# Performance work log

Hardware: AMD Instinct MI355X
Metric: run time of the kernel (lower is better)

## Reference

```python
import jax, jax.numpy as jnp
import numpy as np

N_NODES = 100000
N_EDGES = 1200000
NUM_GRAPHS = 64
D_IN = 64
D_H = 64
D_OUT = 2
BN_EPS = 1e-5


def setup_inputs() -> dict:
    key = jax.random.key(0)
    ks = jax.random.split(key, 12)
    x = jax.random.normal(ks[0], (N_NODES, D_IN), dtype=jnp.float32)
    edge_index = jax.random.randint(ks[1], (2, N_EDGES), 0, N_NODES, dtype=jnp.int64 if jax.config.read('jax_enable_x64') else jnp.int32)
    batch = jnp.sort(jax.random.randint(ks[2], (N_NODES,), 0, NUM_GRAPHS))
    s = 1.0 / np.sqrt(D_H)
    W1 = jax.random.uniform(ks[3], (D_IN, D_H), minval=-s, maxval=s, dtype=jnp.float32)
    b1 = jnp.zeros((D_H,), jnp.float32)
    g1 = jnp.ones((D_H,), jnp.float32); be1 = jnp.zeros((D_H,), jnp.float32)
    m1 = jax.random.normal(ks[4], (D_H,), dtype=jnp.float32) * 0.1
    v1 = jax.random.uniform(ks[5], (D_H,), minval=0.5, maxval=1.5, dtype=jnp.float32)
    W2 = jax.random.uniform(ks[6], (D_H, D_H), minval=-s, maxval=s, dtype=jnp.float32)
    b2 = jnp.zeros((D_H,), jnp.float32)
    g2 = jnp.ones((D_H,), jnp.float32); be2 = jnp.zeros((D_H,), jnp.float32)
    m2 = jax.random.normal(ks[7], (D_H,), dtype=jnp.float32) * 0.1
    v2 = jax.random.uniform(ks[8], (D_H,), minval=0.5, maxval=1.5, dtype=jnp.float32)
    Wc = jax.random.uniform(ks[9], (D_H, D_OUT), minval=-s, maxval=s, dtype=jnp.float32)
    bc = jnp.zeros((D_OUT,), jnp.float32)
    return dict(x=x, edge_index=edge_index, batch=batch, W1=W1, b1=b1, g1=g1, be1=be1, m1=m1, v1=v1,
                W2=W2, b2=b2, g2=g2, be2=be2, m2=m2, v2=v2, Wc=Wc, bc=bc)


def _gcn_conv(x, src, dst, W, b):
    n = x.shape[0]
    h = x @ W  # [N, Dh]
    deg = jax.ops.segment_sum(jnp.ones_like(dst, dtype=h.dtype), dst, num_segments=n)  # includes self-loops
    dinv = jax.lax.rsqrt(jnp.maximum(deg, 1.0))
    norm = dinv[src] * dinv[dst]  # [E+N]
    msg = h[src] * norm[:, None]
    out = jax.ops.segment_sum(msg, dst, num_segments=n)
    return out + b


def _bn(x, g, be, m, v):
    return (x - m) * (g * jax.lax.rsqrt(v + BN_EPS)) + be


def reference(x, edge_index, batch, W1, b1, g1, be1, m1, v1, W2, b2, g2, be2, m2, v2, Wc, bc):
    n = x.shape[0]
    loop = jnp.arange(n, dtype=edge_index.dtype)
    src = jnp.concatenate([edge_index[0], loop])
    dst = jnp.concatenate([edge_index[1], loop])
    h = _gcn_conv(x, src, dst, W1, b1)
    h = jax.nn.relu(_bn(h, g1, be1, m1, v1))  # dropout is identity in eval
    h = _gcn_conv(h, src, dst, W2, b2)
    h = jax.nn.relu(_bn(h, g2, be2, m2, v2))
    # global mean pool over graphs
    sums = jax.ops.segment_sum(h, batch, num_segments=NUM_GRAPHS)
    cnts = jax.ops.segment_sum(jnp.ones((n,), h.dtype), batch, num_segments=NUM_GRAPHS)
    pooled = sums / jnp.maximum(cnts, 1.0)[:, None]
    return pooled @ Wc + bc
```

## Files before the change

### kernel.cpp

```cpp
#include <hip/hip_runtime.h>

#define N_NODES_C 100000
#define N_EDGES_C 1200000
#define NQUADS_C 300000
#define NUM_GRAPHS_C 64
#define D_C 64
#define BN_EPS_C 1e-5f

#define BU_SH 7
#define NB_C 782
#define PART_B 512
#define QPB 586

typedef unsigned short u16;
typedef unsigned int u32;

using frag_ab = __attribute__((ext_vector_type(8))) short;
using f32x4   = __attribute__((ext_vector_type(4))) float;

__device__ __forceinline__ u16 f2bf(float f) {
    u32 x = __float_as_uint(f);
    x += 0x7fffu + ((x >> 16) & 1u);
    return (u16)(x >> 16);
}
__device__ __forceinline__ float bf2f(u16 u) {
    return __uint_as_float(((u32)u) << 16);
}

__global__ void k_prep(const float* __restrict__ x,
                       const float* __restrict__ W1, const float* __restrict__ W2,
                       u16* __restrict__ Xb, u16* __restrict__ Wb1,
                       u16* __restrict__ Wb2, u16* __restrict__ T) {
    int i = blockIdx.x * 256 + threadIdx.x;
    int base = i * 4;
    if (base < N_NODES_C * D_C) {
        float4 f = *(const float4*)(x + base);
        ushort4 o;
        o.x = f2bf(f.x); o.y = f2bf(f.y); o.z = f2bf(f.z); o.w = f2bf(f.w);
        *(ushort4*)(Xb + base) = o;
    }
    if (i < 4096) {
        int n = i >> 6, k = i & 63;
        Wb1[i] = f2bf(W1[k * 64 + n]);
        Wb2[i] = f2bf(W2[k * 64 + n]);
    }
    if (i < 64) T[(size_t)N_NODES_C * 64 + i] = 0;
}


__global__ void __launch_bounds__(256) k_hist(const int* __restrict__ dst,
                                              u32* __restrict__ hist_all) {
    __shared__ u32 hist[NB_C];
    int b = blockIdx.x, t = threadIdx.x;
    for (int i = t; i < NB_C; i += 256) hist[i] = 0;
    __syncthreads();
    int qlo = b * QPB, qhi = qlo + QPB; if (qhi > NQUADS_C) qhi = NQUADS_C;
    const int4* d4 = (const int4*)dst;
    for (int i = qlo + t; i < qhi; i += 256) {
        int4 d = d4[i];
        atomicAdd(&hist[d.x >> BU_SH], 1u);
        atomicAdd(&hist[d.y >> BU_SH], 1u);
        atomicAdd(&hist[d.z >> BU_SH], 1u);
        atomicAdd(&hist[d.w >> BU_SH], 1u);
    }
    __syncthreads();
    for (int i = t; i < NB_C; i += 256) hist_all[(size_t)b * NB_C + i] = hist[i];
}

__global__ void __launch_bounds__(256) k_pscan(const u32* __restrict__ hist_all,
                                               u32* __restrict__ partLocal,
                                               u32* __restrict__ bucketTotal) {
    int wv = blockIdx.x * 4 + (threadIdx.x >> 6);
    int l = threadIdx.x & 63;
    if (wv >= NB_C) return;
    u32 v[8];
#pragma unroll
    for (int j = 0; j < 8; ++j) v[j] = hist_all[(size_t)(l * 8 + j) * NB_C + wv];
    u32 s = 0;
#pragma unroll
    for (int j = 0; j < 8; ++j) { u32 tv = v[j]; v[j] = s; s += tv; }
    u32 run = s;
#pragma unroll
    for (int off = 1; off < 64; off <<= 1) {
        u32 y = __shfl_up(run, off);
        if (l >= off) run += y;
    }
    u32 excl = run - s;
#pragma unroll
    for (int j = 0; j < 8; ++j)
        partLocal[(size_t)(l * 8 + j) * NB_C + wv] = excl + v[j];
    if (l == 63) bucketTotal[wv] = run;
}

__global__ void __launch_bounds__(1024) k_bscan(const u32* __restrict__ bucketTotal,
                                                u32* __restrict__ bucketStart) {
    __shared__ u32 sh[1024];
    int t = threadIdx.x;
    u32 c = (t < NB_C) ? bucketTotal[t] : 0;
    u32 val = c;
    sh[t] = val;
    __syncthreads();
#pragma unroll
    for (int off = 1; off < 1024; off <<= 1) {
        u32 y = (t >= off) ? sh[t - off] : 0;
        __syncthreads();
        val += y;
        sh[t] = val;
        __syncthreads();
    }
    if (t < NB_C) bucketStart[t] = val - c;
    if (t == 0) bucketStart[NB_C] = N_EDGES_C;
}

__global__ void __launch_bounds__(256) k_part(const int* __restrict__ src,
                                              const int* __restrict__ dst,
                                              const u32* __restrict__ partLocal,
                                              const u32* __restrict__ bucketStart,
                                              uint2* __restrict__ pairs) {
    __shared__ u32 baseLDS[NB_C];
    __shared__ u32 rank[NB_C];
    int b = blockIdx.x, t = threadIdx.x;
    for (int i = t; i < NB_C; i += 256) {
        baseLDS[i] = bucketStart[i] + partLocal[(size_t)b * NB_C + i];
        rank[i] = 0;
    }
    __syncthreads();
    int qlo = b * QPB, qhi = qlo + QPB; if (qhi > NQUADS_C) qhi = NQUADS_C;
    const int4* d4 = (const int4*)dst;
    const int4* s4 = (const int4*)src;
    for (int i = qlo + t; i < qhi; i += 256) {
        int4 d = d4[i];
        int4 s = s4[i];
        int dd[4] = {d.x, d.y, d.z, d.w};
        int ss[4] = {s.x, s.y, s.z, s.w};
#pragma unroll
        for (int k = 0; k < 4; ++k) {
            int bu = dd[k] >> BU_SH;
            u32 r = atomicAdd(&rank[bu], 1u);
            pairs[baseLDS[bu] + r] = make_uint2((u32)ss[k], (u32)dd[k]);
        }
    }
}

__global__ void __launch_bounds__(256) k_csr(const uint2* __restrict__ pairs,
                                             const u32* __restrict__ bucketStart,
                                             int* __restrict__ cnt,
                                             int* __restrict__ start,
                                             int* __restrict__ col) {
    __shared__ u32 cl[128];
    __shared__ u32 sl[128];
    __shared__ u32 rk[128];
    __shared__ int sh[256];
    int bu = blockIdx.x, t = threadIdx.x;
    int n0 = bu << BU_SH;
    u32 seg0 = bucketStart[bu], seg1 = bucketStart[bu + 1];
    if (t < 128) { cl[t] = 0; rk[t] = 0; }
    __syncthreads();
    for (u32 i = seg0 + t; i < seg1; i += 256)
        atomicAdd(&cl[pairs[i].y - n0], 1u);
    __syncthreads();
    int c = (t < 128) ? (int)cl[t] : 0;
    int val = c;
    sh[t] = val;
    __syncthreads();
#pragma unroll
    for (int off = 1; off < 128; off <<= 1) {
        int y = (t >= off) ? sh[t - off] : 0;
        __syncthreads();
        val += y;
        sh[t] = val;
        __syncthreads();
    }
    if (t < 128) {
        int node = n0 + t;
        u32 st = seg0 + (u32)(val - c);
        sl[t] = st;
        if (node < N_NODES_C) { cnt[node] = c; start[node] = (int)st; }
    }
    __syncthreads();
    for (u32 i = seg0 + t; i < seg1; i += 256) {
        uint2 pr = pairs[i];
        u32 loc = pr.y - n0;
        u32 r = atomicAdd(&rk[loc], 1u);
        col[sl[loc] + r] = (int)pr.x;
    }
}

__global__ void __launch_bounds__(256) k_gemm_mfma(
        const u16* __restrict__ Xb, const u16* __restrict__ Wb,
        const int* __restrict__ cnt, u16* __restrict__ T) {
    int lane = threadIdx.x & 63;
    int q = lane >> 4, ln = lane & 15;
    int wave = blockIdx.x * 4 + (threadIdx.x >> 6);
    int nwaves = gridDim.x * 4;
    frag_ab bfr[4][2];
#pragma unroll
    for (int nt = 0; nt < 4; ++nt)
#pragma unroll
        for (int kh = 0; kh < 2; ++kh)
            bfr[nt][kh] = *(const frag_ab*)(Wb + (nt * 16 + ln) * 64 + kh * 32 + q * 8);
    const int nstrips = N_NODES_C / 16;
    for (int s = wave; s < nstrips; s += nwaves) {
        int r0 = s * 16;
        frag_ab a0 = *(const frag_ab*)(Xb + (size_t)(r0 + ln) * 64 + q * 8);
        frag_ab a1 = *(const frag_ab*)(Xb + (size_t)(r0 + ln) * 64 + 32 + q * 8);
        f32x4 acc[4];
#pragma unroll
        for (int nt = 0; nt < 4; ++nt) {
            acc[nt] = (f32x4){0.f, 0.f, 0.f, 0.f};
            acc[nt] = __builtin_amdgcn_mfma_f32_16x16x32_bf16(a0, bfr[nt][0], acc[nt], 0, 0, 0);
            acc[nt] = __builtin_amdgcn_mfma_f32_16x16x32_bf16(a1, bfr[nt][1], acc[nt], 0, 0, 0);
        }
        float di[4];
#pragma unroll
        for (int reg = 0; reg < 4; ++reg)
            di[reg] = rsqrtf((float)(cnt[r0 + q * 4 + reg] + 1));
#pragma unroll
        for (int nt = 0; nt < 4; ++nt)
#pragma unroll
            for (int reg = 0; reg < 4; ++reg)
                T[(size_t)(r0 + q * 4 + reg) * 64 + nt * 16 + ln] =
                    f2bf(acc[nt][reg] * di[reg]);
    }
}

template <bool POOL>
__device__ __forceinline__ void gather_body(
        const u16* __restrict__ T, const int* __restrict__ col,
        const int* __restrict__ cnt, const int* __restrict__ start,
        const float* __restrict__ b, const float* __restrict__ g,
        const float* __restrict__ be, const float* __restrict__ m,
        const float* __restrict__ v, const int* __restrict__ batch,
        u16* __restrict__ Ab, float* __restrict__ pooled) {
    const int ZROW = N_NODES_C;
    int lane = threadIdx.x & 63;
    int h = lane >> 4, c = lane & 15;
    int cbase = c << 2;
    int wave = blockIdx.x * 4 + (threadIdx.x >> 6);
    int nwaves = gridDim.x * 4;
    float scv[4], c0v[4];
#pragma unroll
    for (int i = 0; i < 4; ++i) {
        float sci = g[cbase + i] * rsqrtf(v[cbase + i] + BN_EPS_C);
        scv[i] = sci;
        c0v[i] = (b[cbase + i] - m[cbase + i]) * sci + be[cbase + i];
    }
    const int chunk = (N_NODES_C + nwaves - 1) / nwaves;
    int p0 = wave * chunk;
    int p1 = p0 + chunk; if (p1 > N_NODES_C) p1 = N_NODES_C;
    if (p0 >= p1) return;

    float psum = 0.f; int curg = -1;

    int d0 = cnt[p0];
    int s0 = start[p0];
    int d1 = 0, s1 = 0;
    if (p0 + 1 < p1) { d1 = cnt[p0 + 1]; s1 = start[p0 + 1]; }
    int cv0 = col[(size_t)(u32)s0 + lane];

    for (int p = p0; p < p1; ++p) {
        int deg = __builtin_amdgcn_readfirstlane(d0);
        int cvR = cv0;
        if (p + 1 < p1) {
            cv0 = col[(size_t)(u32)s1 + lane];
            d0 = d1;
            if (p + 2 < p1) { d1 = cnt[p + 2]; s1 = start[p + 2]; }
        }
        if (deg > 63) deg = 63;
        int cv = (lane < deg) ? cvR : ((lane == deg) ? p : ZROW);
        int iters = (deg + 4) >> 2;
        float a0 = 0.f, a1 = 0.f, a2 = 0.f, a3 = 0.f;
        int sl = h;
        int j = 0;
        for (; j + 2 <= iters; j += 2) {
            int i0 = __shfl(cv, sl);
            int i1 = __shfl(cv, sl + 4);
            uint2 t0 = *(const uint2*)(T + (((size_t)(u32)i0) << 6) + (c << 2));
            uint2 t1 = *(const uint2*)(T + (((size_t)(u32)i1) << 6) + (c << 2));
            a0 += __uint_as_float(t0.x << 16); a1 += __uint_as_float(t0.x & 0xffff0000u);
            a2 += __uint_as_float(t0.y << 16); a3 += __uint_as_float(t0.y & 0xffff0000u);
            a0 += __uint_as_float(t1.x << 16); a1 += __uint_as_float(t1.x & 0xffff0000u);
            a2 += __uint_as_float(t1.y << 16); a3 += __uint_as_float(t1.y & 0xffff0000u);
            sl += 8;
        }
        if (j < iters) {
            int i0 = __shfl(cv, sl);
            uint2 t0 = *(const uint2*)(T + (((size_t)(u32)i0) << 6) + (c << 2));
            a0 += __uint_as_float(t0.x << 16); a1 += __uint_as_float(t0.x & 0xffff0000u);
            a2 += __uint_as_float(t0.y << 16); a3 += __uint_as_float(t0.y & 0xffff0000u);
        }
        a0 += __shfl_xor(a0, 16); a0 += __shfl_xor(a0, 32);
        a1 += __shfl_xor(a1, 16); a1 += __shfl_xor(a1, 32);
        a2 += __shfl_xor(a2, 16); a2 += __shfl_xor(a2, 32);
        a3 += __shfl_xor(a3, 16); a3 += __shfl_xor(a3, 32);
        float dr = rsqrtf((float)(deg + 1));
        if (POOL) {
            float asel = (h & 2) ? ((h & 1) ? a3 : a2) : ((h & 1) ? a1 : a0);
            float scl  = (h & 2) ? ((h & 1) ? scv[3] : scv[2]) : ((h & 1) ? scv[1] : scv[0]);
            float c0l  = (h & 2) ? ((h & 1) ? c0v[3] : c0v[2]) : ((h & 1) ? c0v[1] : c0v[0]);
            float vh = fmaxf(fmaf(asel * dr, scl, c0l), 0.f);
            int gg = batch[p];
            if (gg != curg) {
                if (curg >= 0) atomicAdd(&pooled[curg * 64 + cbase + h], psum);
                curg = gg; psum = 0.f;
            }
            psum += vh;
        } else {
            float v0 = fmaxf(fmaf(a0 * dr, scv[0], c0v[0]), 0.f);
            float v1 = fmaxf(fmaf(a1 * dr, scv[1], c0v[1]), 0.f);
            float v2 = fmaxf(fmaf(a2 * dr, scv[2], c0v[2]), 0.f);
            float v3 = fmaxf(fmaf(a3 * dr, scv[3], c0v[3]), 0.f);
            if (h == 0) {
                u32 w0 = (u32)f2bf(v0) | ((u32)f2bf(v1) << 16);
                u32 w1 = (u32)f2bf(v2) | ((u32)f2bf(v3) << 16);
                *(uint2*)(Ab + (((size_t)(u32)p) << 6) + (c << 2)) = make_uint2(w0, w1);
            }
        }
    }
    if (POOL && curg >= 0) atomicAdd(&pooled[curg * 64 + cbase + h], psum);
}

__global__ void __launch_bounds__(256) k_gather1(
        const u16* __restrict__ T, const int* __restrict__ col,
        const int* __restrict__ cnt, const int* __restrict__ start,
        const float* __restrict__ b, const float* __restrict__ g,
        const float* __restrict__ be, const float* __restrict__ m,
        const float* __restrict__ v, u16* __restrict__ Ab) {
    gather_body<false>(T, col, cnt, start, b, g, be, m, v, nullptr, Ab, nullptr);
}

__global__ void __launch_bounds__(256) k_gather2(
        const u16* __restrict__ T, const int* __restrict__ col,
        const int* __restrict__ cnt, const int* __restrict__ start,
        const float* __restrict__ b, const float* __restrict__ g,
        const float* __restrict__ be, const float* __restrict__ m,
        const float* __restrict__ v, const int* __restrict__ batch,
        float* __restrict__ pooled) {
    gather_body<true>(T, col, cnt, start, b, g, be, m, v, batch, nullptr, pooled);
}

__global__ void k_final(const float* __restrict__ pooled, const int* __restrict__ batch,
                        const float* __restrict__ Wc, const float* __restrict__ bc,
                        float* __restrict__ out) {
    __shared__ float sp[64 * 65];
    __shared__ int sub[64];
    int t = threadIdx.x;
    for (int i = t; i < 4096; i += 256) sp[(i >> 6) * 65 + (i & 63)] = pooled[i];
    if (t < 64) {
        int lo = 0, hi = N_NODES_C;
        while (lo < hi) { int mid = (lo + hi) >> 1; if (batch[mid] > t) hi = mid; else lo = mid + 1; }
        sub[t] = lo;
    }
    __syncthreads();
    if (t < 64) {
        int gi = t;
        int lb = gi ? sub[gi - 1] : 0;
        int cntg = sub[gi] - lb;
        float inv = 1.0f / fmaxf((float)cntg, 1.0f);
        float a0 = 0.f, a1 = 0.f;
#pragma unroll 8
        for (int f = 0; f < 64; ++f) {
            float p = sp[gi * 65 + f];
            a0 = fmaf(p, Wc[f * 2 + 0], a0);
            a1 = fmaf(p, Wc[f * 2 + 1], a1);
        }
        out[gi * 2 + 0] = a0 * inv + bc[0];
        out[gi * 2 + 1] = a1 * inv + bc[1];
    }
}

extern "C" void kernel_launch(void* const* d_in, const int* in_sizes, int n_in,
                              void* d_out, int out_size, void* d_ws, size_t ws_size,
                              hipStream_t stream) {
    const float* x    = (const float*)d_in[0];
    const int*   ei   = (const int*)d_in[1];
    const int*   batch= (const int*)d_in[2];
    const float* W1 = (const float*)d_in[3];
    const float* b1 = (const float*)d_in[4];
    const float* g1 = (const float*)d_in[5];
    const float* be1= (const float*)d_in[6];
    const float* m1 = (const float*)d_in[7];
    const float* v1 = (const float*)d_in[8];
    const float* W2 = (const float*)d_in[9];
    const float* b2 = (const float*)d_in[10];
    const float* g2 = (const float*)d_in[11];
    const float* be2= (const float*)d_in[12];
    const float* m2 = (const float*)d_in[13];
    const float* v2 = (const float*)d_in[14];
    const float* Wc = (const float*)d_in[15];
    const float* bc = (const float*)d_in[16];
    float* out = (float*)d_out;

    char* ws = (char*)d_ws;
    size_t off = 0;
    auto alloc = [&](size_t bytes) {
        size_t o = off;
        off = (off + bytes + 511) & ~(size_t)511;
        return o;
    };
    size_t o_pool  = alloc((size_t)NUM_GRAPHS_C * D_C * 4);
    size_t zero_bytes = off;
    size_t o_hist  = alloc((size_t)PART_B * NB_C * 4);
    size_t o_ploc  = alloc((size_t)PART_B * NB_C * 4);
    size_t o_btot  = alloc((size_t)NB_C * 4);
    size_t o_bst   = alloc((size_t)(NB_C + 2) * 4);
    size_t o_pairs = alloc((size_t)N_EDGES_C * 8);
    size_t o_cnt   = alloc((size_t)N_NODES_C * 4);
    size_t o_start = alloc((size_t)(N_NODES_C + 64) * 4);
    size_t o_col   = alloc((size_t)(N_EDGES_C + 64) * 4);
    size_t o_xb    = alloc((size_t)N_NODES_C * D_C * 2);
    size_t o_wb1   = alloc(4096 * 2);
    size_t o_wb2   = alloc(4096 * 2);
    size_t o_t     = alloc((size_t)(N_NODES_C + 1) * D_C * 2);
    size_t o_ab    = alloc((size_t)N_NODES_C * D_C * 2);
    (void)ws_size; (void)in_sizes; (void)n_in; (void)out_size;

    float* pooled = (float*)(ws + o_pool);
    u32*   hist   = (u32*)(ws + o_hist);
    u32*   ploc   = (u32*)(ws + o_ploc);
    u32*   btot   = (u32*)(ws + o_btot);
    u32*   bst    = (u32*)(ws + o_bst);
    uint2* pairs  = (uint2*)(ws + o_pairs);
    int*   cnt    = (int*)(ws + o_cnt);
    int*   startp = (int*)(ws + o_start);
    int*   col    = (int*)(ws + o_col);
    u16*   Xb     = (u16*)(ws + o_xb);
    u16*   Wb1    = (u16*)(ws + o_wb1);
    u16*   Wb2    = (u16*)(ws + o_wb2);
    u16*   T      = (u16*)(ws + o_t);
    u16*   Ab     = (u16*)(ws + o_ab);

    const int* srcp = ei;
    const int* dstp = ei + N_EDGES_C;

    hipMemsetAsync(ws, 0, zero_bytes, stream);

    int pblocks = (N_NODES_C * D_C / 4 + 255) / 256;
    int gblocks = 2048;
    int mblocks = 1563;
    k_prep<<<pblocks, 256, 0, stream>>>(x, W1, W2, Xb, Wb1, Wb2, T);
    k_hist<<<PART_B, 256, 0, stream>>>(dstp, hist);
    k_pscan<<<(NB_C + 3) / 4, 256, 0, stream>>>(hist, ploc, btot);
    k_bscan<<<1, 1024, 0, stream>>>(btot, bst);
    k_part<<<PART_B, 256, 0, stream>>>(srcp, dstp, ploc, bst, pairs);
    k_csr<<<NB_C, 256, 0, stream>>>(pairs, bst, cnt, startp, col);

    k_gemm_mfma<<<mblocks, 256, 0, stream>>>(Xb, Wb1, cnt, T);
    k_gather1<<<gblocks, 256, 0, stream>>>(T, col, cnt, startp, b1, g1, be1, m1, v1, Ab);
    k_gemm_mfma<<<mblocks, 256, 0, stream>>>(Ab, Wb2, cnt, T);
    k_gather2<<<gblocks, 256, 0, stream>>>(T, col, cnt, startp, b2, g2, be2, m2, v2,
                                           batch, pooled);
    k_final<<<1, 256, 0, stream>>>(pooled, batch, Wc, bc, out);
}
```

Measured before the change: 235.0 us.

## Fuse fp32-to-bf16 conversion into first GEMM and layer-1 gather with second GEMM

The separate x-to-bf16 pass is removed. The first MFMA GEMM now reads fp32 x and converts it in registers. The layer-1 gather is fused with the second GEMM: each wave aggregates 16 rows into swizzled LDS and then runs the MFMA on them directly, which avoids writing and re-reading the intermediate activation. Edge pairs are packed into 32-bit words (src plus the local dst offset), halving partition traffic, and the partition kernel's block order is permuted. The cost is that the fused gather uses fixed 16-row strips per wave instead of balanced chunks, plus an extra T2 buffer.

```diff
diff --git a/kernel.cpp b/kernel.cpp
--- a/kernel.cpp
+++ b/kernel.cpp
@@ -11,6 +11,7 @@
 #define NB_C 782
 #define PART_B 512
 #define QPB 586
+#define NSTRIP_C 6250
 
 typedef unsigned short u16;
 typedef unsigned int u32;
@@ -27,24 +28,19 @@
     return __uint_as_float(((u32)u) << 16);
 }
 
-__global__ void k_prep(const float* __restrict__ x,
-                       const float* __restrict__ W1, const float* __restrict__ W2,
-                       u16* __restrict__ Xb, u16* __restrict__ Wb1,
-                       u16* __restrict__ Wb2, u16* __restrict__ T) {
+__global__ void k_prepW(const float* __restrict__ W1, const float* __restrict__ W2,
+                        u16* __restrict__ Wb1, u16* __restrict__ Wb2,
+                        u16* __restrict__ T, u16* __restrict__ T2) {
     int i = blockIdx.x * 256 + threadIdx.x;
-    int base = i * 4;
-    if (base < N_NODES_C * D_C) {
-        float4 f = *(const float4*)(x + base);
-        ushort4 o;
-        o.x = f2bf(f.x); o.y = f2bf(f.y); o.z = f2bf(f.z); o.w = f2bf(f.w);
-        *(ushort4*)(Xb + base) = o;
-    }
     if (i < 4096) {
         int n = i >> 6, k = i & 63;
         Wb1[i] = f2bf(W1[k * 64 + n]);
         Wb2[i] = f2bf(W2[k * 64 + n]);
     }
-    if (i < 64) T[(size_t)N_NODES_C * 64 + i] = 0;
+    if (i < 64) {
+        T[(size_t)N_NODES_C * 64 + i] = 0;
+        T2[(size_t)N_NODES_C * 64 + i] = 0;
+    }
 }
 
 
@@ -116,16 +112,17 @@
                                               const int* __restrict__ dst,
                                               const u32* __restrict__ partLocal,
                                               const u32* __restrict__ bucketStart,
-                                              uint2* __restrict__ pairs) {
+                                              u32* __restrict__ pairs) {
     __shared__ u32 baseLDS[NB_C];
     __shared__ u32 rank[NB_C];
-    int b = blockIdx.x, t = threadIdx.x;
+    int lb = ((blockIdx.x & 7) << 6) | (blockIdx.x >> 3);
+    int t = threadIdx.x;
     for (int i = t; i < NB_C; i += 256) {
-        baseLDS[i] = bucketStart[i] + partLocal[(size_t)b * NB_C + i];
+        baseLDS[i] = bucketStart[i] + partLocal[(size_t)lb * NB_C + i];
         rank[i] = 0;
     }
     __syncthreads();
-    int qlo = b * QPB, qhi = qlo + QPB; if (qhi > NQUADS_C) qhi = NQUADS_C;
+    int qlo = lb * QPB, qhi = qlo + QPB; if (qhi > NQUADS_C) qhi = NQUADS_C;
     const int4* d4 = (const int4*)dst;
     const int4* s4 = (const int4*)src;
     for (int i = qlo + t; i < qhi; i += 256) {
@@ -137,12 +134,12 @@
         for (int k = 0; k < 4; ++k) {
             int bu = dd[k] >> BU_SH;
             u32 r = atomicAdd(&rank[bu], 1u);
-            pairs[baseLDS[bu] + r] = make_uint2((u32)ss[k], (u32)dd[k]);
-        }
-    }
-}
-
-__global__ void __launch_bounds__(256) k_csr(const uint2* __restrict__ pairs,
+            pairs[baseLDS[bu] + r] = (u32)ss[k] | ((u32)(dd[k] & 127) << 17);
+        }
+    }
+}
+
+__global__ void __launch_bounds__(256) k_csr(const u32* __restrict__ pairs,
                                              const u32* __restrict__ bucketStart,
                                              int* __restrict__ cnt,
                                              int* __restrict__ start,
@@ -157,7 +154,7 @@
     if (t < 128) { cl[t] = 0; rk[t] = 0; }
     __syncthreads();
     for (u32 i = seg0 + t; i < seg1; i += 256)
-        atomicAdd(&cl[pairs[i].y - n0], 1u);
+        atomicAdd(&cl[pairs[i] >> 17], 1u);
     __syncthreads();
     int c = (t < 128) ? (int)cl[t] : 0;
     int val = c;
@@ -179,65 +176,74 @@
     }
     __syncthreads();
     for (u32 i = seg0 + t; i < seg1; i += 256) {
-        uint2 pr = pairs[i];
-        u32 loc = pr.y - n0;
+        u32 pr = pairs[i];
+        u32 loc = pr >> 17;
         u32 r = atomicAdd(&rk[loc], 1u);
-        col[sl[loc] + r] = (int)pr.x;
-    }
-}
-
-__global__ void __launch_bounds__(256) k_gemm_mfma(
-        const u16* __restrict__ Xb, const u16* __restrict__ Wb,
+        col[sl[loc] + r] = (int)(pr & 0x1ffffu);
+    }
+}
+
+__device__ __forceinline__ frag_ab cvt8(const float* __restrict__ p) {
+    float4 f0 = *(const float4*)p;
+    float4 f1 = *(const float4*)(p + 4);
+    frag_ab r;
+    r[0] = (short)f2bf(f0.x); r[1] = (short)f2bf(f0.y);
+    r[2] = (short)f2bf(f0.z); r[3] = (short)f2bf(f0.w);
+    r[4] = (short)f2bf(f1.x); r[5] = (short)f2bf(f1.y);
+    r[6] = (short)f2bf(f1.z); r[7] = (short)f2bf(f1.w);
+    return r;
+}
+
+__global__ void __launch_bounds__(256) k_xw1(
+        const float* __restrict__ x, const u16* __restrict__ Wb,
         const int* __restrict__ cnt, u16* __restrict__ T) {
     int lane = threadIdx.x & 63;
     int q = lane >> 4, ln = lane & 15;
     int wave = blockIdx.x * 4 + (threadIdx.x >> 6);
-    int nwaves = gridDim.x * 4;
+    if (wave >= NSTRIP_C) return;
     frag_ab bfr[4][2];
 #pragma unroll
     for (int nt = 0; nt < 4; ++nt)
 #pragma unroll
         for (int kh = 0; kh < 2; ++kh)
             bfr[nt][kh] = *(const frag_ab*)(Wb + (nt * 16 + ln) * 64 + kh * 32 + q * 8);
-    const int nstrips = N_NODES_C / 16;
-    for (int s = wave; s < nstrips; s += nwaves) {
-        int r0 = s * 16;
-        frag_ab a0 = *(const frag_ab*)(Xb + (size_t)(r0 + ln) * 64 + q * 8);
-        frag_ab a1 = *(const frag_ab*)(Xb + (size_t)(r0 + ln) * 64 + 32 + q * 8);
-        f32x4 acc[4];
-#pragma unroll
-        for (int nt = 0; nt < 4; ++nt) {
-            acc[nt] = (f32x4){0.f, 0.f, 0.f, 0.f};
-            acc[nt] = __builtin_amdgcn_mfma_f32_16x16x32_bf16(a0, bfr[nt][0], acc[nt], 0, 0, 0);
-            acc[nt] = __builtin_amdgcn_mfma_f32_16x16x32_bf16(a1, bfr[nt][1], acc[nt], 0, 0, 0);
-        }
-        float di[4];
+    int r0 = wave * 16;
+    const float* xr = x + (size_t)(r0 + ln) * 64;
+    frag_ab a0 = cvt8(xr + q * 8);
+    frag_ab a1 = cvt8(xr + 32 + q * 8);
+    f32x4 acc[4];
+#pragma unroll
+    for (int nt = 0; nt < 4; ++nt) {
+        acc[nt] = (f32x4){0.f, 0.f, 0.f, 0.f};
+        acc[nt] = __builtin_amdgcn_mfma_f32_16x16x32_bf16(a0, bfr[nt][0], acc[nt], 0, 0, 0);
+        acc[nt] = __builtin_amdgcn_mfma_f32_16x16x32_bf16(a1, bfr[nt][1], acc[nt], 0, 0, 0);
+    }
+    float di[4];
+#pragma unroll
+    for (int reg = 0; reg < 4; ++reg)
+        di[reg] = rsqrtf((float)(cnt[r0 + q * 4 + reg] + 1));
+#pragma unroll
+    for (int nt = 0; nt < 4; ++nt)
 #pragma unroll
         for (int reg = 0; reg < 4; ++reg)
-            di[reg] = rsqrtf((float)(cnt[r0 + q * 4 + reg] + 1));
-#pragma unroll
-        for (int nt = 0; nt < 4; ++nt)
-#pragma unroll
-            for (int reg = 0; reg < 4; ++reg)
-                T[(size_t)(r0 + q * 4 + reg) * 64 + nt * 16 + ln] =
-                    f2bf(acc[nt][reg] * di[reg]);
-    }
-}
-
-template <bool POOL>
-__device__ __forceinline__ void gather_body(
+            T[(size_t)(r0 + q * 4 + reg) * 64 + nt * 16 + ln] =
+                f2bf(acc[nt][reg] * di[reg]);
+}
+
+__global__ void __launch_bounds__(256) k_g1w2(
         const u16* __restrict__ T, const int* __restrict__ col,
         const int* __restrict__ cnt, const int* __restrict__ start,
+        const u16* __restrict__ Wb2,
         const float* __restrict__ b, const float* __restrict__ g,
         const float* __restrict__ be, const float* __restrict__ m,
-        const float* __restrict__ v, const int* __restrict__ batch,
-        u16* __restrict__ Ab, float* __restrict__ pooled) {
+        const float* __restrict__ v, u16* __restrict__ T2) {
+    __shared__ u16 abuf[4][16][64];
+    __shared__ float dibuf[4][16];
     const int ZROW = N_NODES_C;
     int lane = threadIdx.x & 63;
+    int widx = threadIdx.x >> 6;
     int h = lane >> 4, c = lane & 15;
     int cbase = c << 2;
-    int wave = blockIdx.x * 4 + (threadIdx.x >> 6);
-    int nwaves = gridDim.x * 4;
     float scv[4], c0v[4];
 #pragma unroll
     for (int i = 0; i < 4; ++i) {
@@ -245,26 +251,24 @@
         scv[i] = sci;
         c0v[i] = (b[cbase + i] - m[cbase + i]) * sci + be[cbase + i];
     }
-    const int chunk = (N_NODES_C + nwaves - 1) / nwaves;
-    int p0 = wave * chunk;
-    int p1 = p0 + chunk; if (p1 > N_NODES_C) p1 = N_NODES_C;
-    if (p0 >= p1) return;
-
-    float psum = 0.f; int curg = -1;
-
-    int d0 = cnt[p0];
-    int s0 = start[p0];
-    int d1 = 0, s1 = 0;
-    if (p0 + 1 < p1) { d1 = cnt[p0 + 1]; s1 = start[p0 + 1]; }
+    int wave = blockIdx.x * 4 + widx;
+    if (wave >= NSTRIP_C) return;
+    int r0 = wave * 16;
+    char* ab = (char*)&abuf[widx][0][0];
+
+    int d0 = cnt[r0];
+    int s0 = start[r0];
+    int d1 = cnt[r0 + 1], s1 = start[r0 + 1];
     int cv0 = col[(size_t)(u32)s0 + lane];
 
-    for (int p = p0; p < p1; ++p) {
+    for (int i = 0; i < 16; ++i) {
+        int p = r0 + i;
         int deg = __builtin_amdgcn_readfirstlane(d0);
         int cvR = cv0;
-        if (p + 1 < p1) {
+        if (i + 1 < 16) {
             cv0 = col[(size_t)(u32)s1 + lane];
             d0 = d1;
-            if (p + 2 < p1) { d1 = cnt[p + 2]; s1 = start[p + 2]; }
+            if (i + 2 < 16) { d1 = cnt[p + 2]; s1 = start[p + 2]; }
         }
         if (deg > 63) deg = 63;
         int cv = (lane < deg) ? cvR : ((lane == deg) ? p : ZROW);
@@ -294,39 +298,46 @@
         a2 += __shfl_xor(a2, 16); a2 += __shfl_xor(a2, 32);
         a3 += __shfl_xor(a3, 16); a3 += __shfl_xor(a3, 32);
         float dr = rsqrtf((float)(deg + 1));
-        if (POOL) {
-            float asel = (h & 2) ? ((h & 1) ? a3 : a2) : ((h & 1) ? a1 : a0);
-            float scl  = (h & 2) ? ((h & 1) ? scv[3] : scv[2]) : ((h & 1) ? scv[1] : scv[0]);
-            float c0l  = (h & 2) ? ((h & 1) ? c0v[3] : c0v[2]) : ((h & 1) ? c0v[1] : c0v[0]);
-            float vh = fmaxf(fmaf(asel * dr, scl, c0l), 0.f);
-            int gg = batch[p];
-            if (gg != curg) {
-                if (curg >= 0) atomicAdd(&pooled[curg * 64 + cbase + h], psum);
-                curg = gg; psum = 0.f;
-            }
-            psum += vh;
-        } else {
-            float v0 = fmaxf(fmaf(a0 * dr, scv[0], c0v[0]), 0.f);
-            float v1 = fmaxf(fmaf(a1 * dr, scv[1], c0v[1]), 0.f);
-            float v2 = fmaxf(fmaf(a2 * dr, scv[2], c0v[2]), 0.f);
-            float v3 = fmaxf(fmaf(a3 * dr, scv[3], c0v[3]), 0.f);
-            if (h == 0) {
-                u32 w0 = (u32)f2bf(v0) | ((u32)f2bf(v1) << 16);
-                u32 w1 = (u32)f2bf(v2) | ((u32)f2bf(v3) << 16);
-                *(uint2*)(Ab + (((size_t)(u32)p) << 6) + (c << 2)) = make_uint2(w0, w1);
-            }
-        }
-    }
-    if (POOL && curg >= 0) atomicAdd(&pooled[curg * 64 + cbase + h], psum);
-}
-
-__global__ void __launch_bounds__(256) k_gather1(
-        const u16* __restrict__ T, const int* __restrict__ col,
-        const int* __restrict__ cnt, const int* __restrict__ start,
-        const float* __restrict__ b, const float* __restrict__ g,
-        const float* __restrict__ be, const float* __restrict__ m,
-        const float* __restrict__ v, u16* __restrict__ Ab) {
-    gather_body<false>(T, col, cnt, start, b, g, be, m, v, nullptr, Ab, nullptr);
+        float v0 = fmaxf(fmaf(a0 * dr, scv[0], c0v[0]), 0.f);
+        float v1 = fmaxf(fmaf(a1 * dr, scv[1], c0v[1]), 0.f);
+        float v2 = fmaxf(fmaf(a2 * dr, scv[2], c0v[2]), 0.f);
+        float v3 = fmaxf(fmaf(a3 * dr, scv[3], c0v[3]), 0.f);
+        if (h == 0) {
+            u32 w0 = (u32)f2bf(v0) | ((u32)f2bf(v1) << 16);
+            u32 w1 = (u32)f2bf(v2) | ((u32)f2bf(v3) << 16);
+            int boff = i * 128 + ((c * 8) ^ ((i & 7) << 4));
+            *(uint2*)(ab + boff) = make_uint2(w0, w1);
+            if (c == 0) dibuf[widx][i] = dr;
+        }
+    }
+
+    int q = h, ln = c;
+    frag_ab bfr[4][2];
+#pragma unroll
+    for (int nt = 0; nt < 4; ++nt)
+#pragma unroll
+        for (int kh = 0; kh < 2; ++kh)
+            bfr[nt][kh] = *(const frag_ab*)(Wb2 + (nt * 16 + ln) * 64 + kh * 32 + q * 8);
+    int sw = (ln & 7) << 4;
+    frag_ab fa0 = *(const frag_ab*)(ab + ln * 128 + ((q * 16) ^ sw));
+    frag_ab fa1 = *(const frag_ab*)(ab + ln * 128 + ((64 + q * 16) ^ sw));
+    f32x4 acc[4];
+#pragma unroll
+    for (int nt = 0; nt < 4; ++nt) {
+        acc[nt] = (f32x4){0.f, 0.f, 0.f, 0.f};
+        acc[nt] = __builtin_amdgcn_mfma_f32_16x16x32_bf16(fa0, bfr[nt][0], acc[nt], 0, 0, 0);
+        acc[nt] = __builtin_amdgcn_mfma_f32_16x16x32_bf16(fa1, bfr[nt][1], acc[nt], 0, 0, 0);
+    }
+    float di[4];
+#pragma unroll
+    for (int reg = 0; reg < 4; ++reg)
+        di[reg] = dibuf[widx][q * 4 + reg];
+#pragma unroll
+    for (int nt = 0; nt < 4; ++nt)
+#pragma unroll
+        for (int reg = 0; reg < 4; ++reg)
+            T2[(size_t)(r0 + q * 4 + reg) * 64 + nt * 16 + ln] =
+                f2bf(acc[nt][reg] * di[reg]);
 }
 
 __global__ void __launch_bounds__(256) k_gather2(
@@ -336,7 +347,80 @@
         const float* __restrict__ be, const float* __restrict__ m,
         const float* __restrict__ v, const int* __restrict__ batch,
         float* __restrict__ pooled) {
-    gather_body<true>(T, col, cnt, start, b, g, be, m, v, batch, nullptr, pooled);
+    const int ZROW = N_NODES_C;
+    int lane = threadIdx.x & 63;
+    int h = lane >> 4, c = lane & 15;
+    int cbase = c << 2;
+    int wave = blockIdx.x * 4 + (threadIdx.x >> 6);
+    int nwaves = gridDim.x * 4;
+    float scv[4], c0v[4];
+#pragma unroll
+    for (int i = 0; i < 4; ++i) {
+        float sci = g[cbase + i] * rsqrtf(v[cbase + i] + BN_EPS_C);
+        scv[i] = sci;
+        c0v[i] = (b[cbase + i] - m[cbase + i]) * sci + be[cbase + i];
+    }
+    const int chunk = (N_NODES_C + nwaves - 1) / nwaves;
+    int p0 = wave * chunk;
+    int p1 = p0 + chunk; if (p1 > N_NODES_C) p1 = N_NODES_C;
+    if (p0 >= p1) return;
+
+    float psum = 0.f; int curg = -1;
+
+    int d0 = cnt[p0];
+    int s0 = start[p0];
+    int d1 = 0, s1 = 0;
+    if (p0 + 1 < p1) { d1 = cnt[p0 + 1]; s1 = start[p0 + 1]; }
+    int cv0 = col[(size_t)(u32)s0 + lane];
+
+    for (int p = p0; p < p1; ++p) {
+        int deg = __builtin_amdgcn_readfirstlane(d0);
+        int cvR = cv0;
+        if (p + 1 < p1) {
+            cv0 = col[(size_t)(u32)s1 + lane];
+            d0 = d1;
+            if (p + 2 < p1) { d1 = cnt[p + 2]; s1 = start[p + 2]; }
+        }
+        if (deg > 63) deg = 63;
+        int cv = (lane < deg) ? cvR : ((lane == deg) ? p : ZROW);
+        int iters = (deg + 4) >> 2;
+        float a0 = 0.f, a1 = 0.f, a2 = 0.f, a3 = 0.f;
+        int sl = h;
+        int j = 0;
+        for (; j + 2 <= iters; j += 2) {
+            int i0 = __shfl(cv, sl);
+            int i1 = __shfl(cv, sl + 4);
+            uint2 t0 = *(const uint2*)(T + (((size_t)(u32)i0) << 6) + (c << 2));
+            uint2 t1 = *(const uint2*)(T + (((size_t)(u32)i1) << 6) + (c << 2));
+            a0 += __uint_as_float(t0.x << 16); a1 += __uint_as_float(t0.x & 0xffff0000u);
+            a2 += __uint_as_float(t0.y << 16); a3 += __uint_as_float(t0.y & 0xffff0000u);
+            a0 += __uint_as_float(t1.x << 16); a1 += __uint_as_float(t1.x & 0xffff0000u);
+            a2 += __uint_as_float(t1.y << 16); a3 += __uint_as_float(t1.y & 0xffff0000u);
+            sl += 8;
+        }
+        if (j < iters) {
+            int i0 = __shfl(cv, sl);
+            uint2 t0 = *(const uint2*)(T + (((size_t)(u32)i0) << 6) + (c << 2));
+            a0 += __uint_as_float(t0.x << 16); a1 += __uint_as_float(t0.x & 0xffff0000u);
+            a2 += __uint_as_float(t0.y << 16); a3 += __uint_as_float(t0.y & 0xffff0000u);
+        }
+        a0 += __shfl_xor(a0, 16); a0 += __shfl_xor(a0, 32);
+        a1 += __shfl_xor(a1, 16); a1 += __shfl_xor(a1, 32);
+        a2 += __shfl_xor(a2, 16); a2 += __shfl_xor(a2, 32);
+        a3 += __shfl_xor(a3, 16); a3 += __shfl_xor(a3, 32);
+        float dr = rsqrtf((float)(deg + 1));
+        float asel = (h & 2) ? ((h & 1) ? a3 : a2) : ((h & 1) ? a1 : a0);
+        float scl  = (h & 2) ? ((h & 1) ? scv[3] : scv[2]) : ((h & 1) ? scv[1] : scv[0]);
+        float c0l  = (h & 2) ? ((h & 1) ? c0v[3] : c0v[2]) : ((h & 1) ? c0v[1] : c0v[0]);
+        float vh = fmaxf(fmaf(asel * dr, scl, c0l), 0.f);
+        int gg = batch[p];
+        if (gg != curg) {
+            if (curg >= 0) atomicAdd(&pooled[curg * 64 + cbase + h], psum);
+            curg = gg; psum = 0.f;
+        }
+        psum += vh;
+    }
+    if (curg >= 0) atomicAdd(&pooled[curg * 64 + cbase + h], psum);
 }
 
 __global__ void k_final(const float* __restrict__ pooled, const int* __restrict__ batch,
@@ -404,15 +488,14 @@
     size_t o_ploc  = alloc((size_t)PART_B * NB_C * 4);
     size_t o_btot  = alloc((size_t)NB_C * 4);
     size_t o_bst   = alloc((size_t)(NB_C + 2) * 4);
-    size_t o_pairs = alloc((size_t)N_EDGES_C * 8);
+    size_t o_pairs = alloc((size_t)N_EDGES_C * 4);
     size_t o_cnt   = alloc((size_t)N_NODES_C * 4);
     size_t o_start = alloc((size_t)(N_NODES_C + 64) * 4);
     size_t o_col   = alloc((size_t)(N_EDGES_C + 64) * 4);
-    size_t o_xb    = alloc((size_t)N_NODES_C * D_C * 2);
     size_t o_wb1   = alloc(4096 * 2);
     size_t o_wb2   = alloc(4096 * 2);
     size_t o_t     = alloc((size_t)(N_NODES_C + 1) * D_C * 2);
-    size_t o_ab    = alloc((size_t)N_NODES_C * D_C * 2);
+    size_t o_t2    = alloc((size_t)(N_NODES_C + 1) * D_C * 2);
     (void)ws_size; (void)in_sizes; (void)n_in; (void)out_size;
 
     float* pooled = (float*)(ws + o_pool);
@@ -420,35 +503,33 @@
     u32*   ploc   = (u32*)(ws + o_ploc);
     u32*   btot   = (u32*)(ws + o_btot);
     u32*   bst    = (u32*)(ws + o_bst);
-    uint2* pairs  = (uint2*)(ws + o_pairs);
+    u32*   pairs  = (u32*)(ws + o_pairs);
     int*   cnt    = (int*)(ws + o_cnt);
     int*   startp = (int*)(ws + o_start);
     int*   col    = (int*)(ws + o_col);
-    u16*   Xb     = (u16*)(ws + o_xb);
     u16*   Wb1    = (u16*)(ws + o_wb1);
     u16*   Wb2    = (u16*)(ws + o_wb2);
     u16*   T      = (u16*)(ws + o_t);
-    u16*   Ab     = (u16*)(ws + o_ab);
+    u16*   T2     = (u16*)(ws + o_t2);
 
     const int* srcp = ei;
     const int* dstp = ei + N_EDGES_C;
 
     hipMemsetAsync(ws, 0, zero_bytes, stream);
 
-    int pblocks = (N_NODES_C * D_C / 4 + 255) / 256;
     int gblocks = 2048;
     int mblocks = 1563;
-    k_prep<<<pblocks, 256, 0, stream>>>(x, W1, W2, Xb, Wb1, Wb2, T);
+    k_prepW<<<16, 256, 0, stream>>>(W1, W2, Wb1, Wb2, T, T2);
     k_hist<<<PART_B, 256, 0, stream>>>(dstp, hist);
     k_pscan<<<(NB_C + 3) / 4, 256, 0, stream>>>(hist, ploc, btot);
     k_bscan<<<1, 1024, 0, stream>>>(btot, bst);
     k_part<<<PART_B, 256, 0, stream>>>(srcp, dstp, ploc, bst, pairs);
     k_csr<<<NB_C, 256, 0, stream>>>(pairs, bst, cnt, startp, col);
 
-    k_gemm_mfma<<<mblocks, 256, 0, stream>>>(Xb, Wb1, cnt, T);
-    k_gather1<<<gblocks, 256, 0, stream>>>(T, col, cnt, startp, b1, g1, be1, m1, v1, Ab);
-    k_gemm_mfma<<<mblocks, 256, 0, stream>>>(Ab, Wb2, cnt, T);
-    k_gather2<<<gblocks, 256, 0, stream>>>(T, col, cnt, startp, b2, g2, be2, m2, v2,
+    k_xw1<<<mblocks, 256, 0, stream>>>(x, Wb1, cnt, T);
+    k_g1w2<<<mblocks, 256, 0, stream>>>(T, col, cnt, startp, Wb2,
+                                        b1, g1, be1, m1, v1, T2);
+    k_gather2<<<gblocks, 256, 0, stream>>>(T2, col, cnt, startp, b2, g2, be2, m2, v2,
                                            batch, pooled);
     k_final<<<1, 256, 0, stream>>>(pooled, batch, Wc, bc, out);
 }
```

Result: faster. 217.0 us (-7.7%).
